# Kernel optimization log

Hardware: AMD Instinct MI355X
Metric: run time of the kernel (lower is better)

## Reference

```python
import jax, jax.numpy as jnp
import numpy as np

B, S, D, H = 1, 4096, 1024, 16
HD = D // H  # 64
THETA = 10000.0


def precompute_freqs_cis(dim, end, theta=THETA):
    freqs = 1.0 / theta ** (np.arange(0, dim, 2, dtype=np.float32) / dim)  # [dim//2]
    t = np.arange(end, dtype=np.float32)
    f = np.outer(t, freqs)                       # [end, dim//2]
    f = np.concatenate((f, f), axis=-1)          # [end, dim]
    return jnp.asarray(np.cos(f), jnp.float32), jnp.asarray(np.sin(f), jnp.float32)


def rotate_half(x):
    x1 = x[..., : x.shape[-1] // 2]
    x2 = x[..., x.shape[-1] // 2:]
    return jnp.concatenate((-x2, x1), axis=-1)


def setup_inputs() -> dict:
    key = jax.random.key(0)
    ks = jax.random.split(key, 5)
    x = jax.random.normal(ks[0], (B, S, D), jnp.float32)
    scale = 0.02
    Wq = jax.random.normal(ks[1], (D, H, HD), jnp.float32) * scale
    Wk = jax.random.normal(ks[2], (D, H, HD), jnp.float32) * scale
    Wv = jax.random.normal(ks[3], (D, H, HD), jnp.float32) * scale
    Wo = jax.random.normal(ks[4], (H, HD, D), jnp.float32) * scale
    mask = jnp.tril(jnp.ones((S, S), jnp.bool_))[None, None]  # [1,1,S,S] causal
    return {"x": x, "mask": mask, "Wq": Wq, "Wk": Wk, "Wv": Wv, "Wo": Wo}


def reference(x, mask, Wq, Wk, Wv, Wo):
    # QKV projections: [B,S,D] x [D,H,HD] -> [B,S,H,HD]
    q = jnp.einsum('bsd,dhe->bshe', x, Wq)
    k = jnp.einsum('bsd,dhe->bshe', x, Wk)
    v = jnp.einsum('bsd,dhe->bshe', x, Wv)
    # Rotary position embedding
    cos, sin = precompute_freqs_cis(HD, S)
    cos = cos[None, :, None, :]  # [1,S,1,HD]
    sin = sin[None, :, None, :]
    q = q * cos + rotate_half(q) * sin
    k = k * cos + rotate_half(k) * sin
    # Scaled dot-product attention
    scale = 1.0 / jnp.sqrt(jnp.asarray(HD, jnp.float32))
    scores = jnp.einsum('bqhe,bkhe->bhqk', q * scale, k)  # [B,H,S,S]
    big_neg = jnp.finfo(scores.dtype).min
    scores = jnp.where(mask, scores, big_neg)
    attn = jax.nn.softmax(scores, axis=-1)
    ctx = jnp.einsum('bhqk,bkhe->bqhe', attn, v)  # [B,S,H,HD]
    # Output projection contracting (head, head_dim)
    out = jnp.einsum('bqhe,hed->bqd', ctx, Wo)  # [B,S,D]
    return out
```

## Files before the change

kernel.cpp:

```cpp
#include <hip/hip_runtime.h>
#include <hip/hip_bf16.h>
#include <stdint.h>
#include <stddef.h>

#define S_LEN 4096
#define DMODEL 1024
#define NHEAD 16
#define HDIM 64
#define L2E 1.4426950408889634f
#define FIXED_M 8.0f

typedef __attribute__((ext_vector_type(8))) short bf16x8;
typedef __attribute__((ext_vector_type(8))) unsigned short u16x8;
typedef __attribute__((ext_vector_type(4))) float f32x4;
typedef __attribute__((ext_vector_type(16))) float f32x16;

__device__ __forceinline__ unsigned short f2bf(float f) {
    unsigned int u = __float_as_uint(f);
    return (unsigned short)((u + 0x7FFFu + ((u >> 16) & 1u)) >> 16);
}
__device__ __forceinline__ float bf2f(unsigned short h) {
    return __uint_as_float(((unsigned int)h) << 16);
}

__global__ __launch_bounds__(256) void rope_table_kernel(float* __restrict__ ctab,
                                                         float* __restrict__ stab) {
    int i = blockIdx.x * 256 + threadIdx.x;
    int s = i >> 5, j = i & 31;
    float freq = exp2f(-0.41524101186092407f * (float)j);
    float ang = (float)s * freq;
    ctab[i] = cosf(ang);
    stab[i] = sinf(ang);
}

__global__ __launch_bounds__(256) void cvt_x_kernel(const float* __restrict__ x,
                                                    unsigned short* __restrict__ xb) {
    int i = (blockIdx.x * 256 + threadIdx.x) * 8;
    f32x4 a = *(const f32x4*)(x + i);
    f32x4 b = *(const f32x4*)(x + i + 4);
    u16x8 o;
    #pragma unroll
    for (int j = 0; j < 4; ++j) { o[j] = f2bf(a[j]); o[4 + j] = f2bf(b[j]); }
    *(u16x8*)(xb + i) = o;
}

__global__ __launch_bounds__(256) void cvt_wt_kernel(
    const float* __restrict__ w0, const float* __restrict__ w1,
    const float* __restrict__ w2, const float* __restrict__ w3,
    unsigned short* __restrict__ t0, unsigned short* __restrict__ t1,
    unsigned short* __restrict__ t2, unsigned short* __restrict__ t3) {
    const float* src; unsigned short* dst;
    switch (blockIdx.z) {
        case 0: src = w0; dst = t0; break;
        case 1: src = w1; dst = t1; break;
        case 2: src = w2; dst = t2; break;
        default: src = w3; dst = t3; break;
    }
    __shared__ float tile[64][65];
    int t = threadIdx.x;
    int k0 = blockIdx.y * 64, n0 = blockIdx.x * 64;
    int r = t >> 2, q4 = (t & 3) * 16;
    const float* sp = src + (size_t)(k0 + r) * DMODEL + n0 + q4;
    #pragma unroll
    for (int j = 0; j < 4; ++j) {
        f32x4 v = *(const f32x4*)(sp + j * 4);
        #pragma unroll
        for (int e = 0; e < 4; ++e) tile[r][q4 + j * 4 + e] = v[e];
    }
    __syncthreads();
    int n = t >> 2, kq = (t & 3) * 16;
    unsigned short* dp = dst + (size_t)(n0 + n) * DMODEL + k0 + kq;
    u16x8 a, b;
    #pragma unroll
    for (int j = 0; j < 8; ++j) { a[j] = f2bf(tile[kq + j][n]); b[j] = f2bf(tile[kq + 8 + j][n]); }
    *(u16x8*)dp = a;
    *(u16x8*)(dp + 8) = b;
}

template<int MODE>
__global__ __launch_bounds__(256) void gemm_kernel(
    const unsigned short* __restrict__ Ab,
    const unsigned short* __restrict__ B0,
    const unsigned short* __restrict__ B1,
    const unsigned short* __restrict__ B2,
    unsigned short* __restrict__ o0,
    unsigned short* __restrict__ o1,
    unsigned short* __restrict__ o2,
    float* __restrict__ fo,
    const float* __restrict__ ctab,
    const float* __restrict__ stab) {
    int z = blockIdx.z;
    const unsigned short* Bt = (MODE == 0) ? B0 : (z == 0 ? B0 : (z == 1 ? B1 : B2));
    unsigned short* outp     = (MODE == 0) ? o0 : (z == 0 ? o0 : (z == 1 ? o1 : o2));
    int m0 = blockIdx.y * 128, n0 = blockIdx.x * 128;
    __shared__ unsigned short As[128][72];
    __shared__ unsigned short Bs[128][72];
    int t = threadIdx.x, w = t >> 6, l = t & 63;
    int wm = w >> 1, wn = w & 1, g = l >> 4, c = l & 15;

    f32x4 acc[4][4];
    #pragma unroll
    for (int m = 0; m < 4; ++m)
        #pragma unroll
        for (int n = 0; n < 4; ++n) acc[m][n] = (f32x4){0.f, 0.f, 0.f, 0.f};

    int sr = t >> 1, scc = (t & 1) * 32;

    for (int kt = 0; kt < DMODEL; kt += 64) {
        __syncthreads();
        {
            const unsigned short* gp = Ab + (size_t)(m0 + sr) * DMODEL + kt + scc;
            #pragma unroll
            for (int j = 0; j < 4; ++j)
                *(u16x8*)&As[sr][scc + j * 8] = *(const u16x8*)(gp + j * 8);
        }
        {
            const unsigned short* gp = Bt + (size_t)(n0 + sr) * DMODEL + kt + scc;
            #pragma unroll
            for (int j = 0; j < 4; ++j)
                *(u16x8*)&Bs[sr][scc + j * 8] = *(const u16x8*)(gp + j * 8);
        }
        __syncthreads();
        #pragma unroll
        for (int kk = 0; kk < 64; kk += 32) {
            bf16x8 af[4], bf[4];
            #pragma unroll
            for (int m = 0; m < 4; ++m) af[m] = *(const bf16x8*)&As[wm * 64 + m * 16 + c][kk + g * 8];
            #pragma unroll
            for (int n = 0; n < 4; ++n) bf[n] = *(const bf16x8*)&Bs[wn * 64 + n * 16 + c][kk + g * 8];
            #pragma unroll
            for (int m = 0; m < 4; ++m)
                #pragma unroll
                for (int n = 0; n < 4; ++n)
                    acc[m][n] = __builtin_amdgcn_mfma_f32_16x16x32_bf16(af[m], bf[n], acc[m][n], 0, 0, 0);
        }
    }

    if (MODE == 1 && z < 2) {
        float sc8 = (z == 0) ? 0.125f * L2E : 1.0f;
        #pragma unroll
        for (int m = 0; m < 4; ++m) {
            #pragma unroll
            for (int r = 0; r < 4; ++r) {
                int srow = m0 + wm * 64 + m * 16 + g * 4 + r;
                #pragma unroll
                for (int n = 0; n < 2; ++n) {
                    int e = n * 16 + c;
                    float cs = ctab[srow * 32 + e];
                    float sn = stab[srow * 32 + e];
                    float lo = acc[m][n][r], hi = acc[m][n + 2][r];
                    float nlo = (lo * cs - hi * sn) * sc8;
                    float nhi = (hi * cs + lo * sn) * sc8;
                    size_t base = (size_t)srow * DMODEL + n0 + wn * 64;
                    outp[base + n * 16 + c]       = f2bf(nlo);
                    outp[base + (n + 2) * 16 + c] = f2bf(nhi);
                }
            }
        }
    } else if (MODE == 1) {
        #pragma unroll
        for (int m = 0; m < 4; ++m)
            #pragma unroll
            for (int r = 0; r < 4; ++r) {
                int srow = m0 + wm * 64 + m * 16 + g * 4 + r;
                size_t base = (size_t)srow * DMODEL + n0 + wn * 64;
                #pragma unroll
                for (int n = 0; n < 4; ++n)
                    outp[base + n * 16 + c] = f2bf(acc[m][n][r]);
            }
    } else {
        #pragma unroll
        for (int m = 0; m < 4; ++m)
            #pragma unroll
            for (int r = 0; r < 4; ++r) {
                int srow = m0 + wm * 64 + m * 16 + g * 4 + r;
                size_t base = (size_t)srow * DMODEL + n0 + wn * 64;
                #pragma unroll
                for (int n = 0; n < 4; ++n)
                    fo[base + n * 16 + c] = acc[m][n][r];
            }
    }
}

__global__ __launch_bounds__(512, 4) void attn_kernel(
    const unsigned short* __restrict__ q,
    const unsigned short* __restrict__ k,
    const unsigned short* __restrict__ v,
    unsigned short* __restrict__ Opart,
    float* __restrict__ lpart) {
    int h = blockIdx.x;
    int qb = 31 - (int)blockIdx.y;
    int p = blockIdx.z;
    int t = threadIdx.x, w = t >> 6, l = t & 63, c = l & 31, hi = l >> 5;
    int rg = w & 3, ks = w >> 2;

    __shared__ __align__(16) char smraw[36864];
    unsigned short (*KsT)[64][72] = (unsigned short (*)[64][72])smraw;
    unsigned short (*VtT)[64][72] = (unsigned short (*)[64][72])(smraw + 18432);
    float (*Om)[32][64] = (float (*)[32][64])smraw;
    float* ml           = (float*)(smraw + 32768);

    int qrow = qb * 128 + rg * 32 + c;
    int wrmax = qb * 128 + rg * 32 + 31;

    bf16x8 qf[4];
    {
        const unsigned short* qp = q + (size_t)qrow * DMODEL + h * HDIM + hi * 8;
        #pragma unroll
        for (int s = 0; s < 4; ++s) qf[s] = *(const bf16x8*)(qp + s * 16);
    }

    f32x16 o0, o1;
    #pragma unroll
    for (int i = 0; i < 16; ++i) { o0[i] = 0.f; o1[i] = 0.f; }
    float lsum = 0.f;

    int ts = t & 255;
    int skr = ts >> 2, skc = (ts & 3) * 16;
    int svr = ts & 63, svc = ((ts >> 6) & 3) * 16;
    const unsigned short* gkb = k + (size_t)skr * DMODEL + h * HDIM + skc;
    const unsigned short* gvb = v + (size_t)svr * DMODEL + h * HDIM + svc;

    int NIT = (qb + 2) >> 1;
    int tb = p * (qb + 1);
    u16x8 ka, kb, va, vb;
    if (ks <= qb) {
        size_t off = (size_t)((tb + ks) * 64) * DMODEL;
        ka = *(const u16x8*)(gkb + off);
        kb = *(const u16x8*)(gkb + off + 8);
        va = *(const u16x8*)(gvb + off);
        vb = *(const u16x8*)(gvb + off + 8);
        *(u16x8*)&KsT[ks][skr][skc]     = ka;
        *(u16x8*)&KsT[ks][skr][skc + 8] = kb;
        #pragma unroll
        for (int j = 0; j < 8; ++j) {
            VtT[ks][svc + j][svr]     = va[j];
            VtT[ks][svc + 8 + j][svr] = vb[j];
        }
    }

    for (int it = 0; it < NIT; ++it) {
        int j = 2 * it + ks;
        int kv0 = (tb + j) * 64;
        if (j + 2 <= qb) {
            size_t off = (size_t)(kv0 + 128) * DMODEL;
            ka = *(const u16x8*)(gkb + off);
            kb = *(const u16x8*)(gkb + off + 8);
            va = *(const u16x8*)(gvb + off);
            vb = *(const u16x8*)(gvb + off + 8);
        }
        __syncthreads();

        if (j <= qb) {
            #pragma unroll
            for (int h2 = 0; h2 < 2; ++h2) {
                int kbase = kv0 + h2 * 32;
                if (kbase > wrmax) continue;

                f32x16 sf;
                #pragma unroll
                for (int i = 0; i < 16; ++i) sf[i] = 0.f;
                __builtin_amdgcn_s_setprio(1);
                #pragma unroll
                for (int s = 0; s < 4; ++s) {
                    bf16x8 kf = *(const bf16x8*)&KsT[ks][h2 * 32 + c][s * 16 + hi * 8];
                    sf = __builtin_amdgcn_mfma_f32_32x32x16_bf16(kf, qf[s], sf, 0, 0, 0);
                }
                __builtin_amdgcn_s_setprio(0);

                if (kbase + 31 >= wrmax) {
                    #pragma unroll
                    for (int r = 0; r < 16; ++r) {
                        int key = kbase + (r & 3) + 8 * (r >> 2) + 4 * hi;
                        if (key > qrow) sf[r] = -3.0e38f;
                    }
                }

                float ps = 0.f;
                unsigned int dw[8];
                #pragma unroll
                for (int jj = 0; jj < 8; ++jj) {
                    float p0 = exp2f(sf[2 * jj]     - FIXED_M);
                    float p1 = exp2f(sf[2 * jj + 1] - FIXED_M);
                    ps += p0 + p1;
                    union { struct { __hip_bfloat16 x, y; } h; unsigned int u; } cv;
                    cv.h.x = __float2bfloat16(p0);
                    cv.h.y = __float2bfloat16(p1);
                    dw[jj] = cv.u;
                }
                lsum += ps;

                {
                    auto r0 = __builtin_amdgcn_permlane32_swap(dw[0], dw[2], false, false);
                    dw[0] = r0[0]; dw[2] = r0[1];
                    auto r1 = __builtin_amdgcn_permlane32_swap(dw[1], dw[3], false, false);
                    dw[1] = r1[0]; dw[3] = r1[1];
                    auto r2 = __builtin_amdgcn_permlane32_swap(dw[4], dw[6], false, false);
                    dw[4] = r2[0]; dw[6] = r2[1];
                    auto r3 = __builtin_amdgcn_permlane32_swap(dw[5], dw[7], false, false);
                    dw[5] = r3[0]; dw[7] = r3[1];
                }
                union { unsigned int u[8]; bf16x8 v[2]; } pu;
                #pragma unroll
                for (int jj = 0; jj < 8; ++jj) pu.u[jj] = dw[jj];

                __builtin_amdgcn_s_setprio(1);
                {
                    bf16x8 vf00 = *(const bf16x8*)&VtT[ks][c][h2 * 32 + hi * 8];
                    bf16x8 vf01 = *(const bf16x8*)&VtT[ks][c][h2 * 32 + 16 + hi * 8];
                    bf16x8 vf10 = *(const bf16x8*)&VtT[ks][32 + c][h2 * 32 + hi * 8];
                    bf16x8 vf11 = *(const bf16x8*)&VtT[ks][32 + c][h2 * 32 + 16 + hi * 8];
                    o0 = __builtin_amdgcn_mfma_f32_32x32x16_bf16(pu.v[0], vf00, o0, 0, 0, 0);
                    o0 = __builtin_amdgcn_mfma_f32_32x32x16_bf16(pu.v[1], vf01, o0, 0, 0, 0);
                    o1 = __builtin_amdgcn_mfma_f32_32x32x16_bf16(pu.v[0], vf10, o1, 0, 0, 0);
                    o1 = __builtin_amdgcn_mfma_f32_32x32x16_bf16(pu.v[1], vf11, o1, 0, 0, 0);
                }
                __builtin_amdgcn_s_setprio(0);
            }
        }

        if (it + 1 < NIT) {
            __syncthreads();
            if (j + 2 <= qb) {
                *(u16x8*)&KsT[ks][skr][skc]     = ka;
                *(u16x8*)&KsT[ks][skr][skc + 8] = kb;
                #pragma unroll
                for (int jj = 0; jj < 8; ++jj) {
                    VtT[ks][svc + jj][svr]     = va[jj];
                    VtT[ks][svc + 8 + jj][svr] = vb[jj];
                }
            }
        }
    }

    lsum += __shfl_xor(lsum, 32, 64);

    __syncthreads();
    if (ks == 0) {
        #pragma unroll
        for (int r = 0; r < 16; ++r) {
            int rl = (r & 3) + 8 * (r >> 2) + 4 * hi;
            Om[rg][rl][c]      = o0[r];
            Om[rg][rl][c + 32] = o1[r];
        }
        if (hi == 0) ml[(rg << 5) + c] = lsum;
    }
    __syncthreads();
    if (ks == 1) {
        float lc = ml[(rg << 5) + c] + lsum;
        #pragma unroll
        for (int r = 0; r < 16; ++r) {
            int rl = (r & 3) + 8 * (r >> 2) + 4 * hi;
            int grow = qb * 128 + rg * 32 + rl;
            size_t ob = ((size_t)(p * 16 + h) * 4096 + grow) * 64 + c;
            Opart[ob]      = f2bf(Om[rg][rl][c]      + o0[r]);
            Opart[ob + 32] = f2bf(Om[rg][rl][c + 32] + o1[r]);
        }
        if (hi == 0)
            lpart[(size_t)(p * 16 + h) * 4096 + qrow] = lc;
    }
}

__global__ __launch_bounds__(256) void attn_merge_kernel(
    const unsigned short* __restrict__ Op,
    const float* __restrict__ lp,
    unsigned short* __restrict__ ctx) {
    int i = blockIdx.x * 256 + threadIdx.x;
    int g8 = i & 7;
    int row = (i >> 3) & 4095;
    int h = i >> 15;
    size_t idx = (size_t)h * 4096 + row;
    const size_t PS = (size_t)16 * 4096;
    float inv = 1.0f / (lp[idx] + lp[PS + idx]);
    u16x8 v0 = *(const u16x8*)(Op + idx * 64 + g8 * 8);
    u16x8 v1 = *(const u16x8*)(Op + (PS + idx) * 64 + g8 * 8);
    u16x8 o;
    #pragma unroll
    for (int j = 0; j < 8; ++j)
        o[j] = f2bf((bf2f(v0[j]) + bf2f(v1[j])) * inv);
    *(u16x8*)(ctx + (size_t)row * DMODEL + h * 64 + g8 * 8) = o;
}

extern "C" void kernel_launch(void* const* d_in, const int* in_sizes, int n_in,
                              void* d_out, int out_size, void* d_ws, size_t ws_size,
                              hipStream_t stream) {
    const float* x  = (const float*)d_in[0];
    const float* Wq = (const float*)d_in[2];
    const float* Wk = (const float*)d_in[3];
    const float* Wv = (const float*)d_in[4];
    const float* Wo = (const float*)d_in[5];

    char* ws = (char*)d_ws;
    float* ctab = (float*)(ws);
    float* stab = (float*)(ws + (512u << 10));
    unsigned short* ctx = (unsigned short*)(ws + (1u  << 20));
    unsigned short* Wtq = (unsigned short*)(ws + (1u  << 20));
    unsigned short* Wtk = (unsigned short*)(ws + (3u  << 20));
    unsigned short* Wtv = (unsigned short*)(ws + (5u  << 20));
    unsigned short* Wto = (unsigned short*)(ws + (9u  << 20));
    unsigned short* kr  = (unsigned short*)(ws + (11u << 20));
    unsigned short* vb  = (unsigned short*)(ws + (19u << 20));
    unsigned short* qr  = (unsigned short*)(ws + (27u << 20));
    unsigned short* xb  = (unsigned short*)(ws + (35u << 20));
    unsigned short* Opart = (unsigned short*)(ws + (43u << 20));
    float* lpart = (float*)(ws + (59u << 20));

    rope_table_kernel<<<(S_LEN * 32) / 256, 256, 0, stream>>>(ctab, stab);
    cvt_x_kernel<<<(S_LEN * DMODEL) / 2048, 256, 0, stream>>>(x, xb);
    cvt_wt_kernel<<<dim3(16, 16, 4), 256, 0, stream>>>(Wq, Wk, Wv, Wo, Wtq, Wtk, Wtv, Wto);
    gemm_kernel<1><<<dim3(8, 32, 3), 256, 0, stream>>>(xb, Wtq, Wtk, Wtv,
                                                       qr, kr, vb, nullptr, ctab, stab);
    attn_kernel<<<dim3(16, 32, 2), 512, 0, stream>>>(qr, kr, vb, Opart, lpart);
    attn_merge_kernel<<<(16 * 4096 * 8) / 256, 256, 0, stream>>>(Opart, lpart, ctx);
    gemm_kernel<0><<<dim3(8, 32, 1), 256, 0, stream>>>(ctx, Wto, nullptr, nullptr,
                                                       nullptr, nullptr, nullptr,
                                                       (float*)d_out, ctab, stab);
}
```

Before: 172.0 us.

## Pair short and long query blocks per CTA, finalize short blocks in-kernel

Attention work is rebalanced. Each p==0 block first fully processes a short query block (pair) and writes normalized ctx directly. It then handles the first part of the mirrored long block (31-pair), while the p==1 block handles the remainder. Only the upper half of rows now needs split partials, so the merge kernel shrinks to 2048 rows and the grid halves to 16x16x2. The change trades a longer sequential p==0 block and extra static shared memory (Om/ml no longer aliased with K/V tiles) for fewer launches' worth of partial traffic and better load balance.

```diff
diff --git a/kernel.cpp b/kernel.cpp
--- a/kernel.cpp
+++ b/kernel.cpp
@@ -186,10 +186,11 @@
     const unsigned short* __restrict__ q,
     const unsigned short* __restrict__ k,
     const unsigned short* __restrict__ v,
+    unsigned short* __restrict__ ctx,
     unsigned short* __restrict__ Opart,
     float* __restrict__ lpart) {
     int h = blockIdx.x;
-    int qb = 31 - (int)blockIdx.y;
+    int pair = blockIdx.y;
     int p = blockIdx.z;
     int t = threadIdx.x, w = t >> 6, l = t & 63, c = l & 31, hi = l >> 5;
     int rg = w & 3, ks = w >> 2;
@@ -197,23 +198,8 @@
     __shared__ __align__(16) char smraw[36864];
     unsigned short (*KsT)[64][72] = (unsigned short (*)[64][72])smraw;
     unsigned short (*VtT)[64][72] = (unsigned short (*)[64][72])(smraw + 18432);
-    float (*Om)[32][64] = (float (*)[32][64])smraw;
-    float* ml           = (float*)(smraw + 32768);
-
-    int qrow = qb * 128 + rg * 32 + c;
-    int wrmax = qb * 128 + rg * 32 + 31;
-
-    bf16x8 qf[4];
-    {
-        const unsigned short* qp = q + (size_t)qrow * DMODEL + h * HDIM + hi * 8;
-        #pragma unroll
-        for (int s = 0; s < 4; ++s) qf[s] = *(const bf16x8*)(qp + s * 16);
-    }
-
-    f32x16 o0, o1;
-    #pragma unroll
-    for (int i = 0; i < 16; ++i) { o0[i] = 0.f; o1[i] = 0.f; }
-    float lsum = 0.f;
+    __shared__ float Om[4][32][64];
+    __shared__ float ml[128];
 
     int ts = t & 255;
     int skr = ts >> 2, skc = (ts & 3) * 16;
@@ -221,143 +207,180 @@
     const unsigned short* gkb = k + (size_t)skr * DMODEL + h * HDIM + skc;
     const unsigned short* gvb = v + (size_t)svr * DMODEL + h * HDIM + svc;
 
-    int NIT = (qb + 2) >> 1;
-    int tb = p * (qb + 1);
-    u16x8 ka, kb, va, vb;
-    if (ks <= qb) {
-        size_t off = (size_t)((tb + ks) * 64) * DMODEL;
-        ka = *(const u16x8*)(gkb + off);
-        kb = *(const u16x8*)(gkb + off + 8);
-        va = *(const u16x8*)(gvb + off);
-        vb = *(const u16x8*)(gvb + off + 8);
-        *(u16x8*)&KsT[ks][skr][skc]     = ka;
-        *(u16x8*)&KsT[ks][skr][skc + 8] = kb;
-        #pragma unroll
-        for (int j = 0; j < 8; ++j) {
-            VtT[ks][svc + j][svr]     = va[j];
-            VtT[ks][svc + 8 + j][svr] = vb[j];
-        }
-    }
-
-    for (int it = 0; it < NIT; ++it) {
-        int j = 2 * it + ks;
-        int kv0 = (tb + j) * 64;
-        if (j + 2 <= qb) {
-            size_t off = (size_t)(kv0 + 128) * DMODEL;
+    auto run_segment = [&](int qb, int t0, int cnt, bool finalize) {
+        int qrow = qb * 128 + rg * 32 + c;
+        int wrmax = qb * 128 + rg * 32 + 31;
+
+        bf16x8 qf[4];
+        {
+            const unsigned short* qp = q + (size_t)qrow * DMODEL + h * HDIM + hi * 8;
+            #pragma unroll
+            for (int s = 0; s < 4; ++s) qf[s] = *(const bf16x8*)(qp + s * 16);
+        }
+        f32x16 o0, o1;
+        #pragma unroll
+        for (int i = 0; i < 16; ++i) { o0[i] = 0.f; o1[i] = 0.f; }
+        float lsum = 0.f;
+
+        u16x8 ka, kb, va, vb;
+        if (ks < cnt) {
+            size_t off = (size_t)((t0 + ks) * 64) * DMODEL;
             ka = *(const u16x8*)(gkb + off);
             kb = *(const u16x8*)(gkb + off + 8);
             va = *(const u16x8*)(gvb + off);
             vb = *(const u16x8*)(gvb + off + 8);
-        }
+            *(u16x8*)&KsT[ks][skr][skc]     = ka;
+            *(u16x8*)&KsT[ks][skr][skc + 8] = kb;
+            #pragma unroll
+            for (int j = 0; j < 8; ++j) {
+                VtT[ks][svc + j][svr]     = va[j];
+                VtT[ks][svc + 8 + j][svr] = vb[j];
+            }
+        }
+
+        int NIT = (cnt + 1) >> 1;
+        for (int it = 0; it < NIT; ++it) {
+            int j = 2 * it + ks;
+            int kv0 = (t0 + j) * 64;
+            if (j + 2 < cnt) {
+                size_t off = (size_t)(kv0 + 128) * DMODEL;
+                ka = *(const u16x8*)(gkb + off);
+                kb = *(const u16x8*)(gkb + off + 8);
+                va = *(const u16x8*)(gvb + off);
+                vb = *(const u16x8*)(gvb + off + 8);
+            }
+            __syncthreads();
+
+            if (j < cnt) {
+                #pragma unroll
+                for (int h2 = 0; h2 < 2; ++h2) {
+                    int kbase = kv0 + h2 * 32;
+                    if (kbase > wrmax) continue;
+
+                    f32x16 sf;
+                    #pragma unroll
+                    for (int i = 0; i < 16; ++i) sf[i] = 0.f;
+                    __builtin_amdgcn_s_setprio(1);
+                    #pragma unroll
+                    for (int s = 0; s < 4; ++s) {
+                        bf16x8 kf = *(const bf16x8*)&KsT[ks][h2 * 32 + c][s * 16 + hi * 8];
+                        sf = __builtin_amdgcn_mfma_f32_32x32x16_bf16(kf, qf[s], sf, 0, 0, 0);
+                    }
+                    __builtin_amdgcn_s_setprio(0);
+
+                    if (kbase + 31 >= wrmax) {
+                        #pragma unroll
+                        for (int r = 0; r < 16; ++r) {
+                            int key = kbase + (r & 3) + 8 * (r >> 2) + 4 * hi;
+                            if (key > qrow) sf[r] = -3.0e38f;
+                        }
+                    }
+
+                    float ps = 0.f;
+                    unsigned int dw[8];
+                    #pragma unroll
+                    for (int jj = 0; jj < 8; ++jj) {
+                        float p0 = exp2f(sf[2 * jj]     - FIXED_M);
+                        float p1 = exp2f(sf[2 * jj + 1] - FIXED_M);
+                        ps += p0 + p1;
+                        union { struct { __hip_bfloat16 x, y; } hh; unsigned int u; } cv;
+                        cv.hh.x = __float2bfloat16(p0);
+                        cv.hh.y = __float2bfloat16(p1);
+                        dw[jj] = cv.u;
+                    }
+                    lsum += ps;
+
+                    {
+                        auto r0 = __builtin_amdgcn_permlane32_swap(dw[0], dw[2], false, false);
+                        dw[0] = r0[0]; dw[2] = r0[1];
+                        auto r1 = __builtin_amdgcn_permlane32_swap(dw[1], dw[3], false, false);
+                        dw[1] = r1[0]; dw[3] = r1[1];
+                        auto r2 = __builtin_amdgcn_permlane32_swap(dw[4], dw[6], false, false);
+                        dw[4] = r2[0]; dw[6] = r2[1];
+                        auto r3 = __builtin_amdgcn_permlane32_swap(dw[5], dw[7], false, false);
+                        dw[5] = r3[0]; dw[7] = r3[1];
+                    }
+                    union { unsigned int u[8]; bf16x8 v[2]; } pu;
+                    #pragma unroll
+                    for (int jj = 0; jj < 8; ++jj) pu.u[jj] = dw[jj];
+
+                    __builtin_amdgcn_s_setprio(1);
+                    {
+                        bf16x8 vf00 = *(const bf16x8*)&VtT[ks][c][h2 * 32 + hi * 8];
+                        bf16x8 vf01 = *(const bf16x8*)&VtT[ks][c][h2 * 32 + 16 + hi * 8];
+                        bf16x8 vf10 = *(const bf16x8*)&VtT[ks][32 + c][h2 * 32 + hi * 8];
+                        bf16x8 vf11 = *(const bf16x8*)&VtT[ks][32 + c][h2 * 32 + 16 + hi * 8];
+                        o0 = __builtin_amdgcn_mfma_f32_32x32x16_bf16(pu.v[0], vf00, o0, 0, 0, 0);
+                        o0 = __builtin_amdgcn_mfma_f32_32x32x16_bf16(pu.v[1], vf01, o0, 0, 0, 0);
+                        o1 = __builtin_amdgcn_mfma_f32_32x32x16_bf16(pu.v[0], vf10, o1, 0, 0, 0);
+                        o1 = __builtin_amdgcn_mfma_f32_32x32x16_bf16(pu.v[1], vf11, o1, 0, 0, 0);
+                    }
+                    __builtin_amdgcn_s_setprio(0);
+                }
+            }
+
+            if (it + 1 < NIT) {
+                __syncthreads();
+                if (j + 2 < cnt) {
+                    *(u16x8*)&KsT[ks][skr][skc]     = ka;
+                    *(u16x8*)&KsT[ks][skr][skc + 8] = kb;
+                    #pragma unroll
+                    for (int jj = 0; jj < 8; ++jj) {
+                        VtT[ks][svc + jj][svr]     = va[jj];
+                        VtT[ks][svc + 8 + jj][svr] = vb[jj];
+                    }
+                }
+            }
+        }
+
+        lsum += __shfl_xor(lsum, 32, 64);
+
         __syncthreads();
-
-        if (j <= qb) {
-            #pragma unroll
-            for (int h2 = 0; h2 < 2; ++h2) {
-                int kbase = kv0 + h2 * 32;
-                if (kbase > wrmax) continue;
-
-                f32x16 sf;
-                #pragma unroll
-                for (int i = 0; i < 16; ++i) sf[i] = 0.f;
-                __builtin_amdgcn_s_setprio(1);
-                #pragma unroll
-                for (int s = 0; s < 4; ++s) {
-                    bf16x8 kf = *(const bf16x8*)&KsT[ks][h2 * 32 + c][s * 16 + hi * 8];
-                    sf = __builtin_amdgcn_mfma_f32_32x32x16_bf16(kf, qf[s], sf, 0, 0, 0);
+        if (ks == 0) {
+            #pragma unroll
+            for (int r = 0; r < 16; ++r) {
+                int rl = (r & 3) + 8 * (r >> 2) + 4 * hi;
+                Om[rg][rl][c]      = o0[r];
+                Om[rg][rl][c + 32] = o1[r];
+            }
+            if (hi == 0) ml[(rg << 5) + c] = lsum;
+        }
+        __syncthreads();
+        if (ks == 1) {
+            float lc = ml[(rg << 5) + c] + lsum;
+            if (finalize) {
+                float inv = 1.0f / lc;
+                float invb = __shfl(inv, 0, 1);
+                (void)invb;
+                #pragma unroll
+                for (int r = 0; r < 16; ++r) {
+                    int rl = (r & 3) + 8 * (r >> 2) + 4 * hi;
+                    float invr = __shfl(inv, rl, 32);
+                    int grow = qb * 128 + rg * 32 + rl;
+                    size_t cb = (size_t)grow * DMODEL + h * HDIM + c;
+                    ctx[cb]      = f2bf((Om[rg][rl][c]      + o0[r]) * invr);
+                    ctx[cb + 32] = f2bf((Om[rg][rl][c + 32] + o1[r]) * invr);
                 }
-                __builtin_amdgcn_s_setprio(0);
-
-                if (kbase + 31 >= wrmax) {
-                    #pragma unroll
-                    for (int r = 0; r < 16; ++r) {
-                        int key = kbase + (r & 3) + 8 * (r >> 2) + 4 * hi;
-                        if (key > qrow) sf[r] = -3.0e38f;
-                    }
+            } else {
+                #pragma unroll
+                for (int r = 0; r < 16; ++r) {
+                    int rl = (r & 3) + 8 * (r >> 2) + 4 * hi;
+                    int grow = qb * 128 + rg * 32 + rl;
+                    size_t ob = ((size_t)(p * 16 + h) * 4096 + grow) * 64 + c;
+                    Opart[ob]      = f2bf(Om[rg][rl][c]      + o0[r]);
+                    Opart[ob + 32] = f2bf(Om[rg][rl][c + 32] + o1[r]);
                 }
-
-                float ps = 0.f;
-                unsigned int dw[8];
-                #pragma unroll
-                for (int jj = 0; jj < 8; ++jj) {
-                    float p0 = exp2f(sf[2 * jj]     - FIXED_M);
-                    float p1 = exp2f(sf[2 * jj + 1] - FIXED_M);
-                    ps += p0 + p1;
-                    union { struct { __hip_bfloat16 x, y; } h; unsigned int u; } cv;
-                    cv.h.x = __float2bfloat16(p0);
-                    cv.h.y = __float2bfloat16(p1);
-                    dw[jj] = cv.u;
-                }
-                lsum += ps;
-
-                {
-                    auto r0 = __builtin_amdgcn_permlane32_swap(dw[0], dw[2], false, false);
-                    dw[0] = r0[0]; dw[2] = r0[1];
-                    auto r1 = __builtin_amdgcn_permlane32_swap(dw[1], dw[3], false, false);
-                    dw[1] = r1[0]; dw[3] = r1[1];
-                    auto r2 = __builtin_amdgcn_permlane32_swap(dw[4], dw[6], false, false);
-                    dw[4] = r2[0]; dw[6] = r2[1];
-                    auto r3 = __builtin_amdgcn_permlane32_swap(dw[5], dw[7], false, false);
-                    dw[5] = r3[0]; dw[7] = r3[1];
-                }
-                union { unsigned int u[8]; bf16x8 v[2]; } pu;
-                #pragma unroll
-                for (int jj = 0; jj < 8; ++jj) pu.u[jj] = dw[jj];
-
-                __builtin_amdgcn_s_setprio(1);
-                {
-                    bf16x8 vf00 = *(const bf16x8*)&VtT[ks][c][h2 * 32 + hi * 8];
-                    bf16x8 vf01 = *(const bf16x8*)&VtT[ks][c][h2 * 32 + 16 + hi * 8];
-                    bf16x8 vf10 = *(const bf16x8*)&VtT[ks][32 + c][h2 * 32 + hi * 8];
-                    bf16x8 vf11 = *(const bf16x8*)&VtT[ks][32 + c][h2 * 32 + 16 + hi * 8];
-                    o0 = __builtin_amdgcn_mfma_f32_32x32x16_bf16(pu.v[0], vf00, o0, 0, 0, 0);
-                    o0 = __builtin_amdgcn_mfma_f32_32x32x16_bf16(pu.v[1], vf01, o0, 0, 0, 0);
-                    o1 = __builtin_amdgcn_mfma_f32_32x32x16_bf16(pu.v[0], vf10, o1, 0, 0, 0);
-                    o1 = __builtin_amdgcn_mfma_f32_32x32x16_bf16(pu.v[1], vf11, o1, 0, 0, 0);
-                }
-                __builtin_amdgcn_s_setprio(0);
-            }
-        }
-
-        if (it + 1 < NIT) {
-            __syncthreads();
-            if (j + 2 <= qb) {
-                *(u16x8*)&KsT[ks][skr][skc]     = ka;
-                *(u16x8*)&KsT[ks][skr][skc + 8] = kb;
-                #pragma unroll
-                for (int jj = 0; jj < 8; ++jj) {
-                    VtT[ks][svc + jj][svr]     = va[jj];
-                    VtT[ks][svc + 8 + jj][svr] = vb[jj];
-                }
-            }
-        }
-    }
-
-    lsum += __shfl_xor(lsum, 32, 64);
-
-    __syncthreads();
-    if (ks == 0) {
-        #pragma unroll
-        for (int r = 0; r < 16; ++r) {
-            int rl = (r & 3) + 8 * (r >> 2) + 4 * hi;
-            Om[rg][rl][c]      = o0[r];
-            Om[rg][rl][c + 32] = o1[r];
-        }
-        if (hi == 0) ml[(rg << 5) + c] = lsum;
-    }
-    __syncthreads();
-    if (ks == 1) {
-        float lc = ml[(rg << 5) + c] + lsum;
-        #pragma unroll
-        for (int r = 0; r < 16; ++r) {
-            int rl = (r & 3) + 8 * (r >> 2) + 4 * hi;
-            int grow = qb * 128 + rg * 32 + rl;
-            size_t ob = ((size_t)(p * 16 + h) * 4096 + grow) * 64 + c;
-            Opart[ob]      = f2bf(Om[rg][rl][c]      + o0[r]);
-            Opart[ob + 32] = f2bf(Om[rg][rl][c + 32] + o1[r]);
-        }
-        if (hi == 0)
-            lpart[(size_t)(p * 16 + h) * 4096 + qrow] = lc;
+                if (hi == 0)
+                    lpart[(size_t)(p * 16 + h) * 4096 + qrow] = lc;
+            }
+        }
+    };
+
+    if (p == 0) {
+        run_segment(pair, 0, 2 * pair + 2, true);
+        run_segment(31 - pair, 0, 31 - 2 * pair, false);
+    } else {
+        run_segment(31 - pair, 31 - 2 * pair, 33, false);
     }
 }
 
@@ -367,8 +390,8 @@
     unsigned short* __restrict__ ctx) {
     int i = blockIdx.x * 256 + threadIdx.x;
     int g8 = i & 7;
-    int row = (i >> 3) & 4095;
-    int h = i >> 15;
+    int row = 2048 + ((i >> 3) & 2047);
+    int h = i >> 14;
     size_t idx = (size_t)h * 4096 + row;
     const size_t PS = (size_t)16 * 4096;
     float inv = 1.0f / (lp[idx] + lp[PS + idx]);
@@ -410,8 +433,8 @@
     cvt_wt_kernel<<<dim3(16, 16, 4), 256, 0, stream>>>(Wq, Wk, Wv, Wo, Wtq, Wtk, Wtv, Wto);
     gemm_kernel<1><<<dim3(8, 32, 3), 256, 0, stream>>>(xb, Wtq, Wtk, Wtv,
                                                        qr, kr, vb, nullptr, ctab, stab);
-    attn_kernel<<<dim3(16, 32, 2), 512, 0, stream>>>(qr, kr, vb, Opart, lpart);
-    attn_merge_kernel<<<(16 * 4096 * 8) / 256, 256, 0, stream>>>(Opart, lpart, ctx);
+    attn_kernel<<<dim3(16, 16, 2), 512, 0, stream>>>(qr, kr, vb, ctx, Opart, lpart);
+    attn_merge_kernel<<<(16 * 2048 * 8) / 256, 256, 0, stream>>>(Opart, lpart, ctx);
     gemm_kernel<0><<<dim3(8, 32, 1), 256, 0, stream>>>(ctx, Wto, nullptr, nullptr,
                                                        nullptr, nullptr, nullptr,
                                                        (float*)d_out, ctab, stab);
```

New measurement: 163.4 us. 5.0% less time.
